# Performance work log

Hardware: AMD Instinct MI355X
Metric: run time of the kernel (lower is better)

The kernel has to match this reference:

```python
import jax, jax.numpy as jnp
import numpy as np

N_NODES, N_EDGES, D_IN, D_HID, D_OUT = 50000, 800000, 128, 64, 32


def _glorot(key, shape):
    lim = jnp.sqrt(6.0 / (shape[0] + shape[1]))
    return jax.random.uniform(key, shape, minval=-lim, maxval=lim, dtype=jnp.float32)


def setup_inputs() -> dict:
    key = jax.random.key(0)
    ks = jax.random.split(key, 12)
    return {
        "x": jax.random.normal(ks[0], (N_NODES, D_IN), jnp.float32),
        "edge_index": jax.random.randint(ks[1], (2, N_EDGES), 0, N_NODES, dtype=jnp.int64),
        "edge_weight": jax.random.uniform(ks[2], (N_EDGES,), jnp.float32),
        # layer 1: GATv2Conv(D_IN -> D_HID, heads=1, edge_dim=1)
        "Wl1": _glorot(ks[3], (D_HID, D_IN)), "bl1": jnp.zeros((D_HID,), jnp.float32),
        "Wr1": _glorot(ks[4], (D_HID, D_IN)), "br1": jnp.zeros((D_HID,), jnp.float32),
        "We1": _glorot(ks[5], (D_HID, 1)),
        "att1": _glorot(ks[6], (1, D_HID))[0],
        "bias1": jnp.zeros((D_HID,), jnp.float32),
        # layer 2: GATv2Conv(D_HID -> D_OUT, heads=1, edge_dim=1)
        "Wl2": _glorot(ks[7], (D_OUT, D_HID)), "bl2": jnp.zeros((D_OUT,), jnp.float32),
        "Wr2": _glorot(ks[8], (D_OUT, D_HID)), "br2": jnp.zeros((D_OUT,), jnp.float32),
        "We2": _glorot(ks[9], (D_OUT, 1)),
        "att2": _glorot(ks[10], (1, D_OUT))[0],
        "bias2": jnp.zeros((D_OUT,), jnp.float32),
    }


def _segment_softmax(scores, seg, n):
    m = jax.ops.segment_max(scores, seg, num_segments=n)
    e = jnp.exp(scores - m[seg])
    s = jax.ops.segment_sum(e, seg, num_segments=n)
    return e / s[seg]


def _gatv2(x, src, dst, attr, Wl, bl, Wr, br, We, att, bias, n):
    # PyG GATv2Conv, heads=1, share_weights=False
    xl = x @ Wl.T + bl                    # source transform  [N, D]
    xr = x @ Wr.T + br                    # target transform  [N, D]
    ea = attr @ We.T                      # edge-attr embed   [E, D]
    m = jax.nn.leaky_relu(xl[src] + xr[dst] + ea, negative_slope=0.2)
    score = m @ att                       # [E]
    alpha = _segment_softmax(score, dst, n)
    out = jax.ops.segment_sum(alpha[:, None] * xl[src], dst, num_segments=n)
    return out + bias


def _forward(x, edge_index, edge_weight,
             Wl1, bl1, Wr1, br1, We1, att1, bias1,
             Wl2, bl2, Wr2, br2, We2, att2, bias2):
    n = x.shape[0]
    src, dst = edge_index[0], edge_index[1]
    attr = edge_weight[:, None]           # edge_dim = 1
    # PyG add_self_loops (default True) with fill_value='mean':
    # self-loop attr = mean of incoming edge_attr per node (0 if none)
    cnt = jax.ops.segment_sum(jnp.ones_like(edge_weight), dst, num_segments=n)
    loop_attr = jax.ops.segment_sum(attr, dst, num_segments=n) / jnp.maximum(cnt, 1.0)[:, None]
    loop = jnp.arange(n, dtype=src.dtype)
    src2 = jnp.concatenate([src, loop])
    dst2 = jnp.concatenate([dst, loop])
    attr2 = jnp.concatenate([attr, loop_attr], axis=0)
    h = jax.nn.elu(_gatv2(x, src2, dst2, attr2, Wl1, bl1, Wr1, br1, We1, att1, bias1, n))
    z = _gatv2(h, src2, dst2, attr2, Wl2, bl2, Wr2, br2, We2, att2, bias2, n)
    return jax.nn.softplus(z) + 0.0001


def reference(x, edge_index, edge_weight,
              Wl1, bl1, Wr1, br1, We1, att1, bias1,
              Wl2, bl2, Wr2, br2, We2, att2, bias2):
    return _forward(x, edge_index, edge_weight,
                    Wl1, bl1, Wr1, br1, We1, att1, bias1,
                    Wl2, bl2, Wr2, br2, We2, att2, bias2)
```

## Files before the change

kernel.cpp:

```cpp
#include <hip/hip_runtime.h>
#include <math.h>

typedef unsigned short ushort_t;
typedef __attribute__((ext_vector_type(8))) short bf16x8;
typedef __attribute__((ext_vector_type(4))) float f32x4;

#define NBLK  128
#define MAXNH 25024

template<int CTRL>
__device__ __forceinline__ float dpp_addf(float x)
{
    int y = __builtin_amdgcn_update_dpp(0, __float_as_int(x), CTRL, 0xf, 0xf, true);
    return x + __int_as_float(y);
}

template<int LPE>
__device__ __forceinline__ float group_reduce(float p)
{
    p = dpp_addf<0xB1>(p);
    p = dpp_addf<0x4E>(p);
    if constexpr (LPE >= 8)  p = dpp_addf<0x141>(p);
    if constexpr (LPE >= 16) p = dpp_addf<0x140>(p);
    return p;
}

__device__ __forceinline__ ushort_t f2bf(float f)
{
    unsigned u = __float_as_uint(f);
    return (ushort_t)((u + 0x7fffu + ((u >> 16) & 1u)) >> 16);
}

__global__ __launch_bounds__(256, 1)
void count_hist(const int* __restrict__ ei, ushort_t* __restrict__ lrank,
                ushort_t* __restrict__ histG,
                const float* __restrict__ Wl1, const float* __restrict__ Wr1,
                const float* __restrict__ Wl2, const float* __restrict__ Wr2,
                ushort_t* __restrict__ wab1, ushort_t* __restrict__ wab2,
                int E, int n, int EPB)
{
    const int tid = threadIdx.x;
    const int b   = blockIdx.x;

    if (b == NBLK) {
        for (int k = tid; k < 2 * 64 * 128; k += 256)
            wab1[k] = f2bf(k < 64 * 128 ? Wl1[k] : Wr1[k - 64 * 128]);
        for (int k = tid; k < 2 * 32 * 64; k += 256)
            wab2[k] = f2bf(k < 32 * 64 ? Wl2[k] : Wr2[k - 32 * 64]);
        return;
    }

    __shared__ unsigned h[MAXNH];
    const int nh = (n + 1) >> 1;
    for (int i = tid; i < nh; i += 256) h[i] = 0u;
    __syncthreads();

    const int e0 = b * EPB;
    const int e1 = min(e0 + EPB, E);
    for (int e = e0 + tid; e < e1; e += 256) {
        int d = ei[E + e];
        unsigned sh  = (unsigned)(d & 1) * 16u;
        unsigned old = atomicAdd(&h[d >> 1], 1u << sh);
        lrank[e] = (ushort_t)((old >> sh) & 0xffffu);
    }
    __syncthreads();

    ushort_t* row = histG + (size_t)b * n;
    for (int i = tid; i < n; i += 256) {
        unsigned v = h[i >> 1];
        row[i] = (ushort_t)((v >> ((i & 1) * 16)) & 0xffffu);
    }
}

template<int N, int K>
__global__ __launch_bounds__(256, 2)
void colscan_plus_gemm(ushort_t* __restrict__ histG, int* __restrict__ cnt,
                       int* __restrict__ bsums, int n, int csBlocks,
                       const float* __restrict__ X, const ushort_t* __restrict__ Wab,
                       const float* __restrict__ ba, const float* __restrict__ bb,
                       ushort_t* __restrict__ OutA, ushort_t* __restrict__ OutB,
                       int M)
{
    constexpr int KC = K / 32;
    constexpr int NT = N / 16;
    __shared__ ushort_t sW[N * K];
    __shared__ ushort_t sX[64 * K];
    __shared__ int s[256];
    const int tid = threadIdx.x;

    if (blockIdx.x < csBlocks) {
        int idx = blockIdx.x * 256 + tid;
        unsigned acc = 0;
        if (idx < n) {
            #pragma unroll 1
            for (int b0 = 0; b0 < NBLK; b0 += 16) {
                ushort_t c[16];
                #pragma unroll
                for (int j = 0; j < 16; ++j)
                    c[j] = histG[(size_t)(b0 + j) * n + idx];
                #pragma unroll
                for (int j = 0; j < 16; ++j) {
                    unsigned cc = c[j];
                    histG[(size_t)(b0 + j) * n + idx] = (ushort_t)acc;
                    acc += cc;
                }
            }
            cnt[idx] = (int)acc;
        }
        s[tid] = (idx < n) ? (int)acc : 0;
        __syncthreads();
        #pragma unroll
        for (int off = 128; off >= 1; off >>= 1) {
            if (tid < off) s[tid] += s[tid + off];
            __syncthreads();
        }
        if (tid == 0) bsums[blockIdx.x] = s[0];
        return;
    }

    const int m0 = (blockIdx.x - csBlocks) * 64;

    auto swz = [](int r, int e) {
        return r * K + ((((e >> 3) ^ (r & 7)) << 3) | (e & 7));
    };

    constexpr int WQ8 = N * K / 8;
    for (int q = tid; q < WQ8; q += 256) {
        int nrow = q / (K / 8);
        int e8   = (q % (K / 8)) * 8;
        uint4 v = *(const uint4*)(Wab + (size_t)nrow * K + e8);
        *(uint4*)&sW[swz(nrow, e8)] = v;
    }
    constexpr int XQ = 64 * (K / 4);
    for (int q = tid; q < XQ; q += 256) {
        int r  = q / (K / 4);
        int k4 = (q % (K / 4)) * 4;
        float4 v = make_float4(0.f, 0.f, 0.f, 0.f);
        int gr = m0 + r;
        if (gr < M) v = *(const float4*)(X + (size_t)gr * K + k4);
        short4 h = make_short4((short)f2bf(v.x), (short)f2bf(v.y),
                               (short)f2bf(v.z), (short)f2bf(v.w));
        *(short4*)&sX[swz(r, k4)] = h;
    }
    __syncthreads();

    const int wv   = tid >> 6;
    const int lane = tid & 63;
    const int mrow = lane & 15;
    const int quad = lane >> 4;

    bf16x8 a[KC];
    #pragma unroll
    for (int kc = 0; kc < KC; ++kc)
        a[kc] = *(const bf16x8*)&sX[swz(wv * 16 + mrow, kc * 32 + quad * 8)];

    #pragma unroll
    for (int nt = 0; nt < NT; ++nt) {
        f32x4 acc = {0.f, 0.f, 0.f, 0.f};
        #pragma unroll
        for (int kc = 0; kc < KC; ++kc) {
            bf16x8 bfr = *(const bf16x8*)&sW[swz(nt * 16 + mrow, kc * 32 + quad * 8)];
            acc = __builtin_amdgcn_mfma_f32_16x16x32_bf16(a[kc], bfr, acc, 0, 0, 0);
        }
        const int col = nt * 16 + mrow;
        ushort_t* dst;
        int cc;
        float bv;
        if (col < N / 2) { dst = OutA; cc = col;         bv = ba[cc]; }
        else             { dst = OutB; cc = col - N / 2; bv = bb[cc]; }
        #pragma unroll
        for (int r = 0; r < 4; ++r) {
            int row = m0 + wv * 16 + quad * 4 + r;
            if (row < M)
                dst[(size_t)row * (N / 2) + cc] = f2bf(acc[r] + bv);
        }
    }
}

__global__ __launch_bounds__(256)
void scan_p3(const int* __restrict__ cnt, const int* __restrict__ bsums,
             int* __restrict__ row_off, int n, int nb)
{
    __shared__ int sb[256];
    __shared__ int s[256];
    const int tid = threadIdx.x;

    int bv = (tid < nb) ? bsums[tid] : 0;
    sb[tid] = bv;
    __syncthreads();
    #pragma unroll
    for (int off = 1; off < 256; off <<= 1) {
        int t = (tid >= off) ? sb[tid - off] : 0;
        __syncthreads();
        sb[tid] += t;
        __syncthreads();
    }
    int excl_t = sb[tid] - bv;
    __syncthreads();
    sb[tid] = excl_t;
    __syncthreads();
    const int base = sb[blockIdx.x];

    int gi = blockIdx.x * 256 + tid;
    int c = (gi < n) ? cnt[gi] : 0;
    s[tid] = c;
    __syncthreads();
    #pragma unroll
    for (int off = 1; off < 256; off <<= 1) {
        int t = (tid >= off) ? s[tid - off] : 0;
        __syncthreads();
        s[tid] += t;
        __syncthreads();
    }
    if (gi < n) {
        int excl = base + s[tid] - c;
        row_off[gi] = excl;
        if (gi == n - 1) row_off[n] = excl + c;
    }
}

__global__ __launch_bounds__(256, 1)
void scat_lds(const int* __restrict__ ei, const float* __restrict__ ew,
              const int* __restrict__ row_off, const ushort_t* __restrict__ lrank,
              const ushort_t* __restrict__ boff, int2* __restrict__ slot,
              int E, int n, int EPB)
{
    __shared__ ushort_t sb[2 * MAXNH];
    const int tid = threadIdx.x;
    const int b   = blockIdx.x;

    const ushort_t* row = boff + (size_t)b * n;
    {
        if ((n & 1) == 0 && (((size_t)b * n) & 1) == 0) {
            const unsigned* r32 = (const unsigned*)row;
            unsigned* s32 = (unsigned*)sb;
            for (int i = tid; i < (n >> 1); i += 256) s32[i] = r32[i];
        } else {
            for (int i = tid; i < n; i += 256) sb[i] = row[i];
        }
    }
    __syncthreads();

    const int e0 = b * EPB;
    const int e1 = min(e0 + EPB, E);
    for (int base = e0 + tid; base < e1; base += 256 * 4) {
        int dd[4], ss[4];
        ushort_t rr[4];
        float ww[4];
        #pragma unroll
        for (int j = 0; j < 4; ++j) {
            int e = base + j * 256;
            if (e < e1) {
                dd[j] = ei[E + e];
                rr[j] = lrank[e];
                ss[j] = ei[e];
                ww[j] = ew[e];
            }
        }
        #pragma unroll
        for (int j = 0; j < 4; ++j) {
            int e = base + j * 256;
            if (e < e1) {
                int pos = row_off[dd[j]] + (int)sb[dd[j]] + (int)rr[j];
                slot[pos] = make_int2(ss[j], __float_as_int(ww[j]));
            }
        }
    }
}

template<int N, int K>
__global__ __launch_bounds__(256, 2)
void gemm_xw_mfma(const float* __restrict__ X, const ushort_t* __restrict__ Wab,
                  const float* __restrict__ ba, const float* __restrict__ bb,
                  ushort_t* __restrict__ OutA, ushort_t* __restrict__ OutB, int M)
{
    constexpr int KC = K / 32;
    constexpr int NT = N / 16;
    __shared__ ushort_t sW[N * K];
    __shared__ ushort_t sX[64 * K];
    const int tid = threadIdx.x;
    const int m0  = blockIdx.x * 64;

    auto swz = [](int r, int e) {
        return r * K + ((((e >> 3) ^ (r & 7)) << 3) | (e & 7));
    };

    constexpr int WQ8 = N * K / 8;
    for (int q = tid; q < WQ8; q += 256) {
        int nrow = q / (K / 8);
        int e8   = (q % (K / 8)) * 8;
        uint4 v = *(const uint4*)(Wab + (size_t)nrow * K + e8);
        *(uint4*)&sW[swz(nrow, e8)] = v;
    }
    constexpr int XQ = 64 * (K / 4);
    for (int q = tid; q < XQ; q += 256) {
        int r  = q / (K / 4);
        int k4 = (q % (K / 4)) * 4;
        float4 v = make_float4(0.f, 0.f, 0.f, 0.f);
        int gr = m0 + r;
        if (gr < M) v = *(const float4*)(X + (size_t)gr * K + k4);
        short4 h = make_short4((short)f2bf(v.x), (short)f2bf(v.y),
                               (short)f2bf(v.z), (short)f2bf(v.w));
        *(short4*)&sX[swz(r, k4)] = h;
    }
    __syncthreads();

    const int wv   = tid >> 6;
    const int lane = tid & 63;
    const int mrow = lane & 15;
    const int quad = lane >> 4;

    bf16x8 a[KC];
    #pragma unroll
    for (int kc = 0; kc < KC; ++kc)
        a[kc] = *(const bf16x8*)&sX[swz(wv * 16 + mrow, kc * 32 + quad * 8)];

    #pragma unroll
    for (int nt = 0; nt < NT; ++nt) {
        f32x4 acc = {0.f, 0.f, 0.f, 0.f};
        #pragma unroll
        for (int kc = 0; kc < KC; ++kc) {
            bf16x8 bfr = *(const bf16x8*)&sW[swz(nt * 16 + mrow, kc * 32 + quad * 8)];
            acc = __builtin_amdgcn_mfma_f32_16x16x32_bf16(a[kc], bfr, acc, 0, 0, 0);
        }
        const int col = nt * 16 + mrow;
        ushort_t* dst;
        int cc;
        float bv;
        if (col < N / 2) { dst = OutA; cc = col;         bv = ba[cc]; }
        else             { dst = OutB; cc = col - N / 2; bv = bb[cc]; }
        #pragma unroll
        for (int r = 0; r < 4; ++r) {
            int row = m0 + wv * 16 + quad * 4 + r;
            if (row < M)
                dst[(size_t)row * (N / 2) + cc] = f2bf(acc[r] + bv);
        }
    }
}

template<int D, int ACT>
__global__ __launch_bounds__(256)
void edge_attn(const ushort_t* __restrict__ xl, const ushort_t* __restrict__ xr,
               const float* __restrict__ We, const float* __restrict__ att,
               const float* __restrict__ bias,
               const int* __restrict__ row_off, const int2* __restrict__ slot,
               float* __restrict__ out, int n)
{
    constexpr int LPE = D / 4;
    constexpr int SG  = 64 / LPE;
    const int lane = threadIdx.x & 63;
    const int wid  = threadIdx.x >> 6;
    const int t    = lane % LPE;
    const int g    = lane / LPE;
    const int node = blockIdx.x * 4 + wid;
    if (node >= n) return;

    auto unpack = [](uint2 d) -> float4 {
        float4 r;
        r.x = __uint_as_float(d.x << 16);
        r.y = __uint_as_float(d.x & 0xffff0000u);
        r.z = __uint_as_float(d.y << 16);
        r.w = __uint_as_float(d.y & 0xffff0000u);
        return r;
    };

    const float4 We4   = *(const float4*)(We   + 4 * t);
    const float4 att4  = *(const float4*)(att  + 4 * t);
    const float4 bias4 = *(const float4*)(bias + 4 * t);
    const float4 xr4   = unpack(*(const uint2*)(xr + (size_t)node * D + 4 * t));

    const int start = row_off[node];
    const int end   = row_off[node + 1];
    const int R  = (end - start) / SG;
    const int jt = start + R * SG;
    const bool has_tail = jt < end;

    int2  q[4];
    uint2 xv[4];
    #pragma unroll
    for (int s = 0; s < 4; ++s) {
        if (s < R) {
            q[s]  = slot[start + s * SG + g];
            xv[s] = *(const uint2*)(xl + (size_t)q[s].x * D + 4 * t);
        }
    }
    int2 tq = make_int2(0, 0);
    uint2 tx = make_uint2(0u, 0u);
    if (has_tail) {
        int idx = min(jt + g, end - 1);
        tq = slot[idx];
        tx = *(const uint2*)(xl + (size_t)tq.x * D + 4 * t);
    }
    const uint2 xs = *(const uint2*)(xl + (size_t)node * D + 4 * t);

    float denom = 0.f, wsum = 0.f;
    float4 acc = make_float4(0.f, 0.f, 0.f, 0.f);

    auto body = [&](int2 qe, float4 xvv, bool active) {
        float w = __int_as_float(qe.y);
        float4 v;
        v.x = xvv.x + fmaf(w, We4.x, xr4.x);
        v.y = xvv.y + fmaf(w, We4.y, xr4.y);
        v.z = xvv.z + fmaf(w, We4.z, xr4.z);
        v.w = xvv.w + fmaf(w, We4.w, xr4.w);
        float4 m;
        m.x = fmaxf(v.x, 0.2f * v.x);
        m.y = fmaxf(v.y, 0.2f * v.y);
        m.z = fmaxf(v.z, 0.2f * v.z);
        m.w = fmaxf(v.w, 0.2f * v.w);
        float p = att4.x * m.x + att4.y * m.y + att4.z * m.z + att4.w * m.w;
        p = group_reduce<LPE>(p);
        float e = active ? __expf(p) : 0.f;
        wsum  += active ? w : 0.f;
        denom += e;
        acc.x = fmaf(e, xvv.x, acc.x);
        acc.y = fmaf(e, xvv.y, acc.y);
        acc.z = fmaf(e, xvv.z, acc.z);
        acc.w = fmaf(e, xvv.w, acc.w);
    };

    int b = 0;
    for (; b + 4 <= R; b += 4) {
        #pragma unroll
        for (int s = 0; s < 4; ++s) {
            int2 cq = q[s]; uint2 cx = xv[s];
            int nr = b + 4 + s;
            if (nr < R) {
                q[s]  = slot[start + nr * SG + g];
                xv[s] = *(const uint2*)(xl + (size_t)q[s].x * D + 4 * t);
            }
            body(cq, unpack(cx), true);
        }
    }
    #pragma unroll
    for (int s = 0; s < 4; ++s)
        if (b + s < R) body(q[s], unpack(xv[s]), true);

    if (has_tail)
        body(tq, unpack(tx), (jt + g) < end);

    #pragma unroll
    for (int mask = LPE; mask < 64; mask <<= 1) {
        denom += __shfl_xor(denom, mask);
        wsum  += __shfl_xor(wsum,  mask);
        acc.x += __shfl_xor(acc.x, mask);
        acc.y += __shfl_xor(acc.y, mask);
        acc.z += __shfl_xor(acc.z, mask);
        acc.w += __shfl_xor(acc.w, mask);
    }

    {
        float w = wsum / (float)max(end - start, 1);
        float4 xvs = unpack(xs);
        float4 v;
        v.x = xvs.x + fmaf(w, We4.x, xr4.x);
        v.y = xvs.y + fmaf(w, We4.y, xr4.y);
        v.z = xvs.z + fmaf(w, We4.z, xr4.z);
        v.w = xvs.w + fmaf(w, We4.w, xr4.w);
        float4 m;
        m.x = fmaxf(v.x, 0.2f * v.x);
        m.y = fmaxf(v.y, 0.2f * v.y);
        m.z = fmaxf(v.z, 0.2f * v.z);
        m.w = fmaxf(v.w, 0.2f * v.w);
        float p = att4.x * m.x + att4.y * m.y + att4.z * m.z + att4.w * m.w;
        p = group_reduce<LPE>(p);
        float e = __expf(p);
        denom += e;
        acc.x = fmaf(e, xvs.x, acc.x);
        acc.y = fmaf(e, xvs.y, acc.y);
        acc.z = fmaf(e, xvs.z, acc.z);
        acc.w = fmaf(e, xvs.w, acc.w);
    }

    float4 res;
    res.x = acc.x / denom + bias4.x;
    res.y = acc.y / denom + bias4.y;
    res.z = acc.z / denom + bias4.z;
    res.w = acc.w / denom + bias4.w;
    if (ACT == 0) {
        res.x = fmaxf(res.x, 0.f) + __expf(fminf(res.x, 0.f)) - 1.f;
        res.y = fmaxf(res.y, 0.f) + __expf(fminf(res.y, 0.f)) - 1.f;
        res.z = fmaxf(res.z, 0.f) + __expf(fminf(res.z, 0.f)) - 1.f;
        res.w = fmaxf(res.w, 0.f) + __expf(fminf(res.w, 0.f)) - 1.f;
    } else {
        res.x = fmaxf(res.x, 0.f) + __logf(1.f + __expf(-fabsf(res.x))) + 1e-4f;
        res.y = fmaxf(res.y, 0.f) + __logf(1.f + __expf(-fabsf(res.y))) + 1e-4f;
        res.z = fmaxf(res.z, 0.f) + __logf(1.f + __expf(-fabsf(res.z))) + 1e-4f;
        res.w = fmaxf(res.w, 0.f) + __logf(1.f + __expf(-fabsf(res.w))) + 1e-4f;
    }
    if (g == 0)
        *(float4*)(out + (size_t)node * D + 4 * t) = res;
}

extern "C" void kernel_launch(void* const* d_in, const int* in_sizes, int n_in,
                              void* d_out, int out_size, void* d_ws, size_t ws_size,
                              hipStream_t stream)
{
    const float* x     = (const float*)d_in[0];
    const int*   ei    = (const int*)d_in[1];
    const float* ew    = (const float*)d_in[2];
    const float* Wl1   = (const float*)d_in[3];
    const float* bl1   = (const float*)d_in[4];
    const float* Wr1   = (const float*)d_in[5];
    const float* br1   = (const float*)d_in[6];
    const float* We1   = (const float*)d_in[7];
    const float* att1  = (const float*)d_in[8];
    const float* bias1 = (const float*)d_in[9];
    const float* Wl2   = (const float*)d_in[10];
    const float* bl2   = (const float*)d_in[11];
    const float* Wr2   = (const float*)d_in[12];
    const float* br2   = (const float*)d_in[13];
    const float* We2   = (const float*)d_in[14];
    const float* att2  = (const float*)d_in[15];
    const float* bias2 = (const float*)d_in[16];
    float* out = (float*)d_out;

    const int n = in_sizes[0] / 128;
    const int E = in_sizes[2];
    const int NB = (n + 255) / 256;
    const int EPB = (E + NBLK - 1) / NBLK;
    const int gemmBlocks = (n + 63) / 64;

    char* wp = (char*)d_ws;
    auto carve = [&](size_t bytes) -> void* {
        void* p = (void*)wp;
        wp += (bytes + 255) & ~(size_t)255;
        return p;
    };
    int*      cnt     = (int*)     carve((size_t)n * 4);
    int*      row_off = (int*)     carve((size_t)(n + 1) * 4);
    ushort_t* lrank   = (ushort_t*)carve((size_t)E * 2);
    ushort_t* histG   = (ushort_t*)carve((size_t)NBLK * n * 2);
    int*      bsums   = (int*)     carve((size_t)256 * 4);
    int2*     slot    = (int2*)    carve((size_t)E * 8);
    ushort_t* wab1    = (ushort_t*)carve((size_t)2 * 64 * 128 * 2);
    ushort_t* wab2    = (ushort_t*)carve((size_t)2 * 32 * 64 * 2);
    ushort_t* xl1     = (ushort_t*)carve((size_t)n * 64 * 2);
    ushort_t* xr1     = (ushort_t*)carve((size_t)n * 64 * 2);
    float*    hbuf    = (float*)   carve((size_t)n * 64 * 4);
    ushort_t* xl2     = (ushort_t*)carve((size_t)n * 32 * 2);
    ushort_t* xr2     = (ushort_t*)carve((size_t)n * 32 * 2);

    count_hist<<<NBLK + 1, 256, 0, stream>>>(ei, lrank, histG,
                                             Wl1, Wr1, Wl2, Wr2, wab1, wab2,
                                             E, n, EPB);
    colscan_plus_gemm<128, 128><<<NB + gemmBlocks, 256, 0, stream>>>(
        histG, cnt, bsums, n, NB, x, wab1, bl1, br1, xl1, xr1, n);
    scan_p3<<<NB, 256, 0, stream>>>(cnt, bsums, row_off, n, NB);
    scat_lds<<<NBLK, 256, 0, stream>>>(ei, ew, row_off, lrank, histG, slot,
                                       E, n, EPB);

    edge_attn<64, 0><<<(n + 3) / 4, 256, 0, stream>>>(xl1, xr1, We1, att1, bias1,
                                                      row_off, slot, hbuf, n);
    gemm_xw_mfma<64, 64><<<(n + 63) / 64, 256, 0, stream>>>(hbuf, wab2, bl2, br2,
                                                            xl2, xr2, n);
    edge_attn<32, 1><<<(n + 3) / 4, 256, 0, stream>>>(xl2, xr2, We2, att2, bias2,
                                                      row_off, slot, out, n);
}
```

Measured before the change: 241.9 us.

## Split histogram and scatter blocks by destination-node halves to double block count

Each edge chunk is now handled by two blocks, each owning half of the destination-node range in LDS, for both the counting histogram and the scatter kernel. This halves per-block LDS use so two blocks fit per CU and 256 blocks fill more of the GPU. In exchange every block reads all destination indices of its chunk and discards half, which doubles the dst-index reads.

```diff
diff --git a/kernel.cpp b/kernel.cpp
--- a/kernel.cpp
+++ b/kernel.cpp
@@ -6,7 +6,8 @@
 typedef __attribute__((ext_vector_type(4))) float f32x4;
 
 #define NBLK  128
-#define MAXNH 25024
+#define HNH   12512
+#define HNS   25024
 
 template<int CTRL>
 __device__ __forceinline__ float dpp_addf(float x)
@@ -31,7 +32,7 @@
     return (ushort_t)((u + 0x7fffu + ((u >> 16) & 1u)) >> 16);
 }
 
-__global__ __launch_bounds__(256, 1)
+__global__ __launch_bounds__(256, 2)
 void count_hist(const int* __restrict__ ei, ushort_t* __restrict__ lrank,
                 ushort_t* __restrict__ histG,
                 const float* __restrict__ Wl1, const float* __restrict__ Wr1,
@@ -40,9 +41,9 @@
                 int E, int n, int EPB)
 {
     const int tid = threadIdx.x;
-    const int b   = blockIdx.x;
-
-    if (b == NBLK) {
+    const int bb  = blockIdx.x;
+
+    if (bb == 2 * NBLK) {
         for (int k = tid; k < 2 * 64 * 128; k += 256)
             wab1[k] = f2bf(k < 64 * 128 ? Wl1[k] : Wr1[k - 64 * 128]);
         for (int k = tid; k < 2 * 32 * 64; k += 256)
@@ -50,8 +51,14 @@
         return;
     }
 
-    __shared__ unsigned h[MAXNH];
-    const int nh = (n + 1) >> 1;
+    const int b    = bb >> 1;
+    const int half = bb & 1;
+    const int H    = (n + 1) >> 1;
+    const int h0   = half * H;
+    const int span = min(h0 + H, n) - h0;
+
+    __shared__ unsigned h[HNH];
+    const int nh = (span + 1) >> 1;
     for (int i = tid; i < nh; i += 256) h[i] = 0u;
     __syncthreads();
 
@@ -59,14 +66,17 @@
     const int e1 = min(e0 + EPB, E);
     for (int e = e0 + tid; e < e1; e += 256) {
         int d = ei[E + e];
-        unsigned sh  = (unsigned)(d & 1) * 16u;
-        unsigned old = atomicAdd(&h[d >> 1], 1u << sh);
-        lrank[e] = (ushort_t)((old >> sh) & 0xffffu);
-    }
-    __syncthreads();
-
-    ushort_t* row = histG + (size_t)b * n;
-    for (int i = tid; i < n; i += 256) {
+        unsigned li = (unsigned)(d - h0);
+        if (li < (unsigned)span) {
+            unsigned sh  = (li & 1) * 16u;
+            unsigned old = atomicAdd(&h[li >> 1], 1u << sh);
+            lrank[e] = (ushort_t)((old >> sh) & 0xffffu);
+        }
+    }
+    __syncthreads();
+
+    ushort_t* row = histG + (size_t)b * n + h0;
+    for (int i = tid; i < span; i += 256) {
         unsigned v = h[i >> 1];
         row[i] = (ushort_t)((v >> ((i & 1) * 16)) & 0xffffu);
     }
@@ -219,39 +229,49 @@
     }
 }
 
-__global__ __launch_bounds__(256, 1)
+__global__ __launch_bounds__(256, 2)
 void scat_lds(const int* __restrict__ ei, const float* __restrict__ ew,
               const int* __restrict__ row_off, const ushort_t* __restrict__ lrank,
               const ushort_t* __restrict__ boff, int2* __restrict__ slot,
               int E, int n, int EPB)
 {
-    __shared__ ushort_t sb[2 * MAXNH];
-    const int tid = threadIdx.x;
-    const int b   = blockIdx.x;
-
-    const ushort_t* row = boff + (size_t)b * n;
-    {
-        if ((n & 1) == 0 && (((size_t)b * n) & 1) == 0) {
-            const unsigned* r32 = (const unsigned*)row;
-            unsigned* s32 = (unsigned*)sb;
-            for (int i = tid; i < (n >> 1); i += 256) s32[i] = r32[i];
-        } else {
-            for (int i = tid; i < n; i += 256) sb[i] = row[i];
-        }
+    __shared__ ushort_t sb[HNS];
+    const int tid  = threadIdx.x;
+    const int bb   = blockIdx.x;
+    const int b    = bb >> 1;
+    const int half = bb & 1;
+    const int H    = (n + 1) >> 1;
+    const int h0   = half * H;
+    const int span = min(h0 + H, n) - h0;
+
+    const ushort_t* row = boff + (size_t)b * n + h0;
+    if (((((size_t)b * n + h0) & 1) == 0) && ((span & 1) == 0)) {
+        const unsigned* r32 = (const unsigned*)row;
+        unsigned* s32 = (unsigned*)sb;
+        for (int i = tid; i < (span >> 1); i += 256) s32[i] = r32[i];
+    } else {
+        for (int i = tid; i < span; i += 256) sb[i] = row[i];
     }
     __syncthreads();
 
     const int e0 = b * EPB;
     const int e1 = min(e0 + EPB, E);
     for (int base = e0 + tid; base < e1; base += 256 * 4) {
-        int dd[4], ss[4];
+        int dd[4];
+        bool act[4];
+        #pragma unroll
+        for (int j = 0; j < 4; ++j) {
+            int e = base + j * 256;
+            dd[j]  = (e < e1) ? ei[E + e] : 0;
+            act[j] = (e < e1) && ((unsigned)(dd[j] - h0) < (unsigned)span);
+        }
+        int ss[4];
         ushort_t rr[4];
         float ww[4];
         #pragma unroll
         for (int j = 0; j < 4; ++j) {
             int e = base + j * 256;
-            if (e < e1) {
-                dd[j] = ei[E + e];
+            if (act[j]) {
                 rr[j] = lrank[e];
                 ss[j] = ei[e];
                 ww[j] = ew[e];
@@ -259,9 +279,8 @@
         }
         #pragma unroll
         for (int j = 0; j < 4; ++j) {
-            int e = base + j * 256;
-            if (e < e1) {
-                int pos = row_off[dd[j]] + (int)sb[dd[j]] + (int)rr[j];
+            if (act[j]) {
+                int pos = row_off[dd[j]] + (int)sb[dd[j] - h0] + (int)rr[j];
                 slot[pos] = make_int2(ss[j], __float_as_int(ww[j]));
             }
         }
@@ -541,14 +560,14 @@
     ushort_t* xl2     = (ushort_t*)carve((size_t)n * 32 * 2);
     ushort_t* xr2     = (ushort_t*)carve((size_t)n * 32 * 2);
 
-    count_hist<<<NBLK + 1, 256, 0, stream>>>(ei, lrank, histG,
-                                             Wl1, Wr1, Wl2, Wr2, wab1, wab2,
-                                             E, n, EPB);
+    count_hist<<<2 * NBLK + 1, 256, 0, stream>>>(ei, lrank, histG,
+                                                 Wl1, Wr1, Wl2, Wr2, wab1, wab2,
+                                                 E, n, EPB);
     colscan_plus_gemm<128, 128><<<NB + gemmBlocks, 256, 0, stream>>>(
         histG, cnt, bsums, n, NB, x, wab1, bl1, br1, xl1, xr1, n);
     scan_p3<<<NB, 256, 0, stream>>>(cnt, bsums, row_off, n, NB);
-    scat_lds<<<NBLK, 256, 0, stream>>>(ei, ew, row_off, lrank, histG, slot,
-                                       E, n, EPB);
+    scat_lds<<<2 * NBLK, 256, 0, stream>>>(ei, ew, row_off, lrank, histG, slot,
+                                           E, n, EPB);
 
     edge_attn<64, 0><<<(n + 3) / 4, 256, 0, stream>>>(xl1, xr1, We1, att1, bias1,
                                                       row_off, slot, hbuf, n);
```

New measurement: 240.6 us, median of 2. No clear change (-0.5%).
